# Kernel optimization log

Measured on AMD Instinct MI355X. Metric: run time of the kernel, lower is better.

Reference implementation:

```python
import jax, jax.numpy as jnp
import numpy as np

N_HEADS = 16
D_MODEL = 1024
D_K = D_MODEL // N_HEADS
B, S = 2, 2048


def setup_inputs() -> dict:
    key = jax.random.key(0)
    ks = jax.random.split(key, 12)
    sc = 1.0 / np.sqrt(D_MODEL)
    inp = {
        'query': jax.random.normal(ks[0], (B, S, D_MODEL), jnp.float32),
        'key':   jax.random.normal(ks[1], (B, S, D_MODEL), jnp.float32),
        'value': jax.random.normal(ks[2], (B, S, D_MODEL), jnp.float32),
        'mask':  jnp.ones((B, 1, 1, S), jnp.int32),
        'Wq': jax.random.normal(ks[3], (D_MODEL, D_MODEL), jnp.float32) * sc,
        'bq': jnp.zeros((D_MODEL,), jnp.float32),
        'Wk': jax.random.normal(ks[4], (D_MODEL, D_MODEL), jnp.float32) * sc,
        'bk': jnp.zeros((D_MODEL,), jnp.float32),
        'Wv': jax.random.normal(ks[5], (D_MODEL, D_MODEL), jnp.float32) * sc,
        'bv': jnp.zeros((D_MODEL,), jnp.float32),
        'Wo': jax.random.normal(ks[6], (D_MODEL, D_MODEL), jnp.float32) * sc,
        'bo': jnp.zeros((D_MODEL,), jnp.float32),
    }
    return inp


def reference(query, key, value, mask, Wq, bq, Wk, bk, Wv, bv, Wo, bo):
    # Linear projections (torch Linear: x @ W.T + b)
    q = query @ Wq.T + bq
    k = key @ Wk.T + bk
    v = value @ Wv.T + bv
    # [B, S, D] -> [B, H, S, d_k]
    def split_heads(x):
        b, s, _ = x.shape
        return x.reshape(b, s, N_HEADS, D_K).transpose(0, 2, 1, 3)
    q, k, v = split_heads(q), split_heads(k), split_heads(v)
    # scaled dot-product attention with explicit [B,H,S,S] scores
    att = jnp.einsum('bhqd,bhkd->bhqk', q, k) / jnp.sqrt(jnp.float32(D_K))
    att = jnp.where(mask == 0, -jnp.inf, att)
    scores = jax.nn.softmax(att, axis=-1)
    # dropout is identity in eval/reference mode
    out = jnp.einsum('bhqk,bhkd->bhqd', scores, v)
    b = out.shape[0]
    out = out.transpose(0, 2, 1, 3).reshape(b, -1, N_HEADS * D_K)
    return out @ Wo.T + bo
```

## Files before the change

kernel.cpp:

```cpp
#include <hip/hip_runtime.h>
#include <hip/hip_bf16.h>

#define DM   1024
#define SLEN 2048
#define NH   16
#define DK   64

typedef float f32x4 __attribute__((ext_vector_type(4)));
typedef short short8 __attribute__((ext_vector_type(8)));
typedef short short4v __attribute__((ext_vector_type(4)));

__device__ __forceinline__ unsigned short f2bf(float f) {
  union { float f; unsigned int u; } x; x.f = f;
  unsigned int r = x.u + 0x7fffu + ((x.u >> 16) & 1u);
  return (unsigned short)(r >> 16);
}

__device__ __forceinline__ void gload_lds16(const unsigned short* g, unsigned short* l) {
  __builtin_amdgcn_global_load_lds(
      (const __attribute__((address_space(1))) unsigned int*)g,
      (__attribute__((address_space(3))) unsigned int*)l, 16, 0, 0);
}

__device__ __forceinline__ f32x4 mfma32(short8 a, short8 b, f32x4 c) {
  return __builtin_amdgcn_mfma_f32_16x16x32_bf16(a, b, c, 0, 0, 0);
}

__device__ __forceinline__ f32x4 mfma16(short4v a, short4v b, f32x4 c) {
#if __has_builtin(__builtin_amdgcn_mfma_f32_16x16x16bf16_1k)
  return __builtin_amdgcn_mfma_f32_16x16x16bf16_1k(a, b, c, 0, 0, 0);
#else
  f32x4 d;
  asm volatile("v_mfma_f32_16x16x16_bf16 %0, %1, %2, %3"
               : "=v"(d) : "v"(a), "v"(b), "v"(c));
  return d;
#endif
}

struct ConvArgs { const float* src[7]; unsigned short* dst[7]; };

__global__ __launch_bounds__(256) void conv_kernel(ConvArgs a) {
  int blk = blockIdx.x, seg, base;
  if (blk < 6144) { seg = blk >> 11; base = blk & 2047; }
  else { int t = blk - 6144; seg = 3 + (t >> 9); base = t & 511; }
  const float* s = a.src[seg];
  unsigned short* d = a.dst[seg];
  int idx = (base * 256 + (int)threadIdx.x) * 8;
  float4 v0 = *(const float4*)(s + idx);
  float4 v1 = *(const float4*)(s + idx + 4);
  unsigned short o[8];
  o[0]=f2bf(v0.x); o[1]=f2bf(v0.y); o[2]=f2bf(v0.z); o[3]=f2bf(v0.w);
  o[4]=f2bf(v1.x); o[5]=f2bf(v1.y); o[6]=f2bf(v1.z); o[7]=f2bf(v1.w);
  *(uint4*)(d + idx) = *(uint4*)o;
}

__device__ __forceinline__ void gemm_core(int mode,
                                          const unsigned short* __restrict__ A,
                                          const unsigned short* __restrict__ W,
                                          const float* __restrict__ bias,
                                          void* __restrict__ outp, float scale,
                                          int m0, int n0, char* smem) {
  unsigned short* As = (unsigned short*)smem;
  unsigned short* Bs = (unsigned short*)(smem + 16384);
  const int tid = threadIdx.x;
  const int lane = tid & 63;
  const int l15 = lane & 15;
  const int quad = lane >> 4;
  const int wv = tid >> 6;
  const int wm = (wv >> 1) * 64, wn = (wv & 1) * 32;

  f32x4 acc[4][2];
#pragma unroll
  for (int i = 0; i < 4; ++i)
#pragma unroll
    for (int j = 0; j < 2; ++j) acc[i][j] = (f32x4){0.f, 0.f, 0.f, 0.f};

  for (int k0 = 0; k0 < DM; k0 += 64) {
    __syncthreads();
#pragma unroll
    for (int i = 0; i < 4; ++i) {
      int c = tid + i * 256;
      int row = c >> 3, sc = ((c & 7) ^ (row & 7)) << 3;
      gload_lds16(A + (size_t)(m0 + row) * DM + k0 + sc, As + c * 8);
    }
#pragma unroll
    for (int i = 0; i < 2; ++i) {
      int c = tid + i * 256;
      int row = c >> 3, sc = ((c & 7) ^ (row & 7)) << 3;
      gload_lds16(W + (size_t)(n0 + row) * DM + k0 + sc, Bs + c * 8);
    }
    __syncthreads();
    short8 af[4][2], bf[2][2];
#pragma unroll
    for (int i = 0; i < 4; ++i) {
      int r = wm + i * 16 + l15;
#pragma unroll
      for (int kf = 0; kf < 2; ++kf)
        af[i][kf] = *(const short8*)(As + r * 64 + (((kf * 4 + quad) ^ (r & 7)) << 3));
    }
#pragma unroll
    for (int j = 0; j < 2; ++j) {
      int r = wn + j * 16 + l15;
#pragma unroll
      for (int kf = 0; kf < 2; ++kf)
        bf[j][kf] = *(const short8*)(Bs + r * 64 + (((kf * 4 + quad) ^ (r & 7)) << 3));
    }
#pragma unroll
    for (int kf = 0; kf < 2; ++kf)
#pragma unroll
      for (int i = 0; i < 4; ++i)
#pragma unroll
        for (int j = 0; j < 2; ++j)
          acc[i][j] = mfma32(af[i][kf], bf[j][kf], acc[i][j]);
  }

  const int hh = n0 >> 6;
  const int brow = m0 >> 11;
  const int srow0 = m0 & (SLEN - 1);

  if (mode == 0) {
    __syncthreads();
    unsigned short* Ls = (unsigned short*)smem;
#pragma unroll
    for (int i = 0; i < 4; ++i)
#pragma unroll
      for (int j = 0; j < 2; ++j) {
        int dloc = wn + j * 16 + l15;
        float bv = bias[n0 + dloc];
        int sl = wm + i * 16 + quad * 4;
#pragma unroll
        for (int g = 0; g < 4; ++g)
          Ls[(sl + g) * 66 + dloc] = f2bf((acc[i][j][g] + bv) * scale);
      }
    __syncthreads();
    unsigned short* gout = (unsigned short*)outp +
        ((size_t)(brow * NH + hh) * SLEN + srow0) * DK;
    int sl = tid >> 1, dch = (tid & 1) * 32;
#pragma unroll
    for (int k = 0; k < 4; ++k)
      *(uint4*)(gout + (size_t)sl * DK + dch + k * 8) =
          *(const uint4*)(Ls + sl * 66 + dch + k * 8);
  } else if (mode == 2) {
    __syncthreads();
    unsigned short* Ls = (unsigned short*)smem;
#pragma unroll
    for (int i = 0; i < 4; ++i)
#pragma unroll
      for (int j = 0; j < 2; ++j) {
        int dloc = wn + j * 16 + l15;
        float bv = bias[n0 + dloc];
        int sl = wm + i * 16 + quad * 4;
#pragma unroll
        for (int g = 0; g < 4; ++g)
          Ls[dloc * 132 + sl + g] = f2bf(acc[i][j][g] + bv);
      }
    __syncthreads();
    unsigned short* gout = (unsigned short*)outp +
        (size_t)(brow * NH + hh) * DK * SLEN + srow0;
    int dloc = tid >> 2, sch = (tid & 3) * 32;
#pragma unroll
    for (int k = 0; k < 4; ++k)
      *(uint4*)(gout + (size_t)dloc * SLEN + sch + k * 8) =
          *(const uint4*)(Ls + dloc * 132 + sch + k * 8);
  } else {
    float* Lf = (float*)smem;
#pragma unroll
    for (int hf = 0; hf < 2; ++hf) {
      __syncthreads();
      if ((wv >> 1) == hf) {
#pragma unroll
        for (int i = 0; i < 4; ++i)
#pragma unroll
          for (int j = 0; j < 2; ++j) {
            int dloc = wn + j * 16 + l15;
            float bv = bias[n0 + dloc];
            int sl = i * 16 + quad * 4;
#pragma unroll
            for (int g = 0; g < 4; ++g)
              Lf[(sl + g) * 68 + dloc] = acc[i][j][g] + bv;
          }
      }
      __syncthreads();
      int row = tid >> 2, cch = (tid & 3) * 16;
      float* gout = (float*)outp + (size_t)(m0 + hf * 64 + row) * DM + n0 + cch;
#pragma unroll
      for (int k = 0; k < 4; ++k)
        *(float4*)(gout + k * 4) = *(const float4*)(Lf + row * 68 + cch + k * 4);
    }
  }
}

struct QKVArgs {
  const unsigned short* A[3];
  const unsigned short* W[3];
  const float* bias[3];
  unsigned short* out[3];
  float scale[3];
  int mode[3];
};

__global__ __launch_bounds__(256, 4) void gemm_qkv_kernel(QKVArgs a) {
  __shared__ char smem[24576];
  int z = blockIdx.z, bid = blockIdx.x;
  int xm = (bid & 7) + ((bid >> 7) << 3);
  int yn = (bid >> 3) & 15;
  gemm_core(a.mode[z], a.A[z], a.W[z], a.bias[z], a.out[z], a.scale[z],
            xm * 128, yn * 64, smem);
}

__global__ __launch_bounds__(256, 4) void gemm_o_kernel(const unsigned short* __restrict__ A,
                                                        const unsigned short* __restrict__ W,
                                                        const float* __restrict__ bias,
                                                        float* __restrict__ out) {
  __shared__ char smem[24576];
  int bid = blockIdx.x;
  int xm = (bid & 7) + ((bid >> 7) << 3);
  int yn = (bid >> 3) & 15;
  gemm_core(1, A, W, bias, out, 1.0f, xm * 128, yn * 64, smem);
}

__global__ __launch_bounds__(512, 4) void attn_kernel(
    const unsigned short* __restrict__ Qw,
    const unsigned short* __restrict__ Kw,
    const unsigned short* __restrict__ Vtw,
    const int* __restrict__ mask,
    unsigned short* __restrict__ attn_out) {
  __shared__ uint4 smem4[4160];
  char* smb = (char*)smem4;
  float* Oex = (float*)smb;
  float* lsX = (float*)(smb + 33024);

  const int tid = threadIdx.x;
  const int lane = tid & 63;
  const int l15 = lane & 15;
  const int quad = lane >> 4;
  const int wv = tid >> 6;
  const int grp = wv >> 2;
  const int widx = wv & 3;
  const int tg = tid & 255;

  const int bid = blockIdx.x;
  const int bh = (bid & 7) + ((bid >> 7) << 3);
  const int s0 = ((bid >> 3) & 15) * 128;
  const int b = bh >> 4, h = bh & 15;
  const unsigned short* Qb = Qw + (size_t)bh * (SLEN * DK);
  const unsigned short* Kb = Kw + (size_t)bh * (SLEN * DK);
  const unsigned short* Vtb = Vtw + (size_t)bh * (SLEN * DK);

  const int qb = widx * 32;
  short8 bq[2][2];
#pragma unroll
  for (int qt = 0; qt < 2; ++qt)
#pragma unroll
    for (int kf = 0; kf < 2; ++kf)
      bq[qt][kf] = *(const short8*)(Qb + (size_t)(s0 + qb + qt * 16 + l15) * DK + kf * 32 + quad * 8);

  const int c0 = tg, c1 = tg + 256;
  const int r0c = c0 >> 3, s0c = ((c0 & 7) ^ (r0c & 7)) << 3;
  const int r1c = c1 >> 3, s1c = ((c1 & 7) ^ (r1c & 7)) << 3;

  {
    unsigned short* K0 = (unsigned short*)(smb + grp * 8192);
    unsigned short* V0 = (unsigned short*)(smb + 32768 + grp * 8192);
    int kv0 = grp * 64;
    gload_lds16(Kb + (size_t)(kv0 + r0c) * DK + s0c, K0 + c0 * 8);
    gload_lds16(Kb + (size_t)(kv0 + r1c) * DK + s1c, K0 + c1 * 8);
    gload_lds16(Vtb + (size_t)r0c * SLEN + kv0 + s0c, V0 + c0 * 8);
    gload_lds16(Vtb + (size_t)r1c * SLEN + kv0 + s1c, V0 + c1 * 8);
  }
  int mreg = 1;
  if (tg < 64) {
    ((float*)(smb + 65536 + grp * 256))[tg] = mask[b * SLEN + grp * 64 + tg] ? 0.0f : -1e30f;
    mreg = mask[b * SLEN + (2 + grp) * 64 + tg];
  }
  __syncthreads();

  f32x4 O[4][2];
#pragma unroll
  for (int dt = 0; dt < 4; ++dt)
#pragma unroll
    for (int qt = 0; qt < 2; ++qt) O[dt][qt] = (f32x4){0.f, 0.f, 0.f, 0.f};
  float lsum[2] = {0.f, 0.f};

  int cb = 0;
  for (int it = 0; it < 16; ++it) {
    const int nb = cb ^ 1;
    if (it < 15) {
      unsigned short* Kn = (unsigned short*)(smb + grp * 8192 + nb * 16384);
      unsigned short* Vn = (unsigned short*)(smb + 32768 + grp * 8192 + nb * 16384);
      int kvn = ((it + 1) * 2 + grp) * 64;
      gload_lds16(Kb + (size_t)(kvn + r0c) * DK + s0c, Kn + c0 * 8);
      gload_lds16(Kb + (size_t)(kvn + r1c) * DK + s1c, Kn + c1 * 8);
      gload_lds16(Vtb + (size_t)r0c * SLEN + kvn + s0c, Vn + c0 * 8);
      gload_lds16(Vtb + (size_t)r1c * SLEN + kvn + s1c, Vn + c1 * 8);
      if (tg < 64) {
        ((float*)(smb + 65536 + nb * 512 + grp * 256))[tg] = mreg ? 0.0f : -1e30f;
        if (it < 14) mreg = mask[b * SLEN + ((it + 2) * 2 + grp) * 64 + tg];
      }
    }

    unsigned short* KstG = (unsigned short*)(smb + grp * 8192 + cb * 16384);
    unsigned short* VstG = (unsigned short*)(smb + 32768 + grp * 8192 + cb * 16384);
    float* maskG = (float*)(smb + 65536 + cb * 512 + grp * 256);

    f32x4 st[4][2];
#pragma unroll
    for (int ct = 0; ct < 4; ++ct) {
      int r = ct * 16 + l15;
      short8 ka0 = *(const short8*)(KstG + r * 64 + ((quad ^ (r & 7)) << 3));
      short8 ka1 = *(const short8*)(KstG + r * 64 + (((4 + quad) ^ (r & 7)) << 3));
#pragma unroll
      for (int qt = 0; qt < 2; ++qt) {
        f32x4 z = (f32x4){0.f, 0.f, 0.f, 0.f};
        z = mfma32(ka0, bq[qt][0], z);
        st[ct][qt] = mfma32(ka1, bq[qt][1], z);
      }
    }
    short4v pf[4][2];
#pragma unroll
    for (int ct = 0; ct < 4; ++ct) {
      f32x4 ma = *(const f32x4*)(maskG + ct * 16 + quad * 4);
#pragma unroll
      for (int qt = 0; qt < 2; ++qt) {
        float p0 = __builtin_exp2f(st[ct][qt][0] + ma[0]);
        float p1 = __builtin_exp2f(st[ct][qt][1] + ma[1]);
        float p2 = __builtin_exp2f(st[ct][qt][2] + ma[2]);
        float p3 = __builtin_exp2f(st[ct][qt][3] + ma[3]);
        lsum[qt] += (p0 + p1) + (p2 + p3);
        union { short4v s; __hip_bfloat162 h[2]; } u;
        u.h[0] = __float22bfloat162_rn(float2{p0, p1});
        u.h[1] = __float22bfloat162_rn(float2{p2, p3});
        pf[ct][qt] = u.s;
      }
    }
#pragma unroll
    for (int dt = 0; dt < 4; ++dt) {
      int rd = dt * 16 + l15;
      short4v vf[4];
#pragma unroll
      for (int ct = 0; ct < 4; ++ct) {
        int slot = (ct * 2 + (quad >> 1)) ^ (rd & 7);
        vf[ct] = *(const short4v*)(VstG + rd * 64 + slot * 8 + (quad & 1) * 4);
      }
#pragma unroll
      for (int qt = 0; qt < 2; ++qt)
#pragma unroll
        for (int ct = 0; ct < 4; ++ct)
          O[dt][qt] = mfma16(vf[ct], pf[ct][qt], O[dt][qt]);
    }
    __syncthreads();
    cb = nb;
  }

#pragma unroll
  for (int qt = 0; qt < 2; ++qt) {
    lsum[qt] += __shfl_xor(lsum[qt], 16);
    lsum[qt] += __shfl_xor(lsum[qt], 32);
  }
  if (grp == 1) {
#pragma unroll
    for (int dt = 0; dt < 4; ++dt)
#pragma unroll
      for (int qt = 0; qt < 2; ++qt) {
        int qg = qb + qt * 16 + l15;
#pragma unroll
        for (int i = 0; i < 4; ++i)
          Oex[(dt * 16 + quad * 4 + i) * 129 + qg] = O[dt][qt][i];
      }
    if (quad == 0) {
      lsX[qb + lane] = lsum[0];
      lsX[qb + 16 + lane] = lsum[1];
    }
  }
  __syncthreads();
  if (grp == 0) {
#pragma unroll
    for (int qt = 0; qt < 2; ++qt) {
      int qg = qb + qt * 16 + l15;
      float inv = 1.0f / (lsum[qt] + lsX[qg]);
      int srow = s0 + qg;
#pragma unroll
      for (int dt = 0; dt < 4; ++dt) {
        int d0 = dt * 16 + quad * 4;
        unsigned short pk[4];
#pragma unroll
        for (int i = 0; i < 4; ++i)
          pk[i] = f2bf((O[dt][qt][i] + Oex[(d0 + i) * 129 + qg]) * inv);
        *(uint2*)(attn_out + (size_t)(b * SLEN + srow) * DM + h * DK + d0) = *(uint2*)pk;
      }
    }
  }
}

extern "C" void kernel_launch(void* const* d_in, const int* in_sizes, int n_in,
                              void* d_out, int out_size, void* d_ws, size_t ws_size,
                              hipStream_t stream) {
  (void)in_sizes; (void)n_in; (void)out_size; (void)ws_size;
  const float* query = (const float*)d_in[0];
  const float* key_  = (const float*)d_in[1];
  const float* value = (const float*)d_in[2];
  const int*   mask  = (const int*)d_in[3];
  const float* Wq = (const float*)d_in[4];
  const float* bq = (const float*)d_in[5];
  const float* Wk = (const float*)d_in[6];
  const float* bk = (const float*)d_in[7];
  const float* Wv = (const float*)d_in[8];
  const float* bv = (const float*)d_in[9];
  const float* Wo = (const float*)d_in[10];
  const float* bo = (const float*)d_in[11];
  float* out = (float*)d_out;

  const size_t WSZ = 1048576, XSZ = 4194304;
  unsigned short* base = (unsigned short*)d_ws;
  unsigned short* Wqb = base;
  unsigned short* Wkb = base + WSZ;
  unsigned short* Wvb = base + 2 * WSZ;
  unsigned short* Wob = base + 3 * WSZ;
  unsigned short* Xqb = base + 4 * WSZ;
  unsigned short* Xkb = Xqb + XSZ;
  unsigned short* Xvb = Xqb + 2 * XSZ;
  unsigned short* Qw  = Xqb + 3 * XSZ;
  unsigned short* Kw  = Qw + XSZ;
  unsigned short* Vtw = Qw + 2 * XSZ;
  unsigned short* attnb = Qw + 3 * XSZ;

  ConvArgs ca;
  ca.src[0] = query; ca.src[1] = key_; ca.src[2] = value;
  ca.src[3] = Wq; ca.src[4] = Wk; ca.src[5] = Wv; ca.src[6] = Wo;
  ca.dst[0] = Xqb; ca.dst[1] = Xkb; ca.dst[2] = Xvb;
  ca.dst[3] = Wqb; ca.dst[4] = Wkb; ca.dst[5] = Wvb; ca.dst[6] = Wob;
  conv_kernel<<<8192, 256, 0, stream>>>(ca);

  QKVArgs qa;
  qa.A[0] = Xqb; qa.A[1] = Xkb; qa.A[2] = Xvb;
  qa.W[0] = Wqb; qa.W[1] = Wkb; qa.W[2] = Wvb;
  qa.bias[0] = bq; qa.bias[1] = bk; qa.bias[2] = bv;
  qa.out[0] = Qw; qa.out[1] = Kw; qa.out[2] = Vtw;
  qa.scale[0] = 0.18033688011112042f;
  qa.scale[1] = 1.0f; qa.scale[2] = 1.0f;
  qa.mode[0] = 0; qa.mode[1] = 0; qa.mode[2] = 2;
  gemm_qkv_kernel<<<dim3(512, 1, 3), 256, 0, stream>>>(qa);

  attn_kernel<<<dim3(512), 512, 0, stream>>>(Qw, Kw, Vtw, mask, attnb);

  gemm_o_kernel<<<dim3(512), 256, 0, stream>>>(attnb, Wob, bo, out);
}
```

Measured before the change: 250.6 us.

## Enlarge GEMM tiles to 128x128, shrink K-step, and register-stage attention K/V loads

```diff
diff --git a/kernel.cpp b/kernel.cpp
--- a/kernel.cpp
+++ b/kernel.cpp
@@ -61,131 +61,129 @@
                                           void* __restrict__ outp, float scale,
                                           int m0, int n0, char* smem) {
   unsigned short* As = (unsigned short*)smem;
-  unsigned short* Bs = (unsigned short*)(smem + 16384);
+  unsigned short* Bs = (unsigned short*)(smem + 8192);
   const int tid = threadIdx.x;
   const int lane = tid & 63;
   const int l15 = lane & 15;
   const int quad = lane >> 4;
   const int wv = tid >> 6;
-  const int wm = (wv >> 1) * 64, wn = (wv & 1) * 32;
-
-  f32x4 acc[4][2];
+  const int wm = (wv >> 1) * 64, wn = (wv & 1) * 64;
+
+  f32x4 acc[4][4];
 #pragma unroll
   for (int i = 0; i < 4; ++i)
 #pragma unroll
-    for (int j = 0; j < 2; ++j) acc[i][j] = (f32x4){0.f, 0.f, 0.f, 0.f};
-
-  for (int k0 = 0; k0 < DM; k0 += 64) {
+    for (int j = 0; j < 4; ++j) acc[i][j] = (f32x4){0.f, 0.f, 0.f, 0.f};
+
+  const int crow = tid >> 2, coff = (tid & 3) << 3;
+  const int crow2 = (tid + 256) >> 2, coff2 = ((tid + 256) & 3) << 3;
+
+  for (int k0 = 0; k0 < DM; k0 += 32) {
     __syncthreads();
-#pragma unroll
-    for (int i = 0; i < 4; ++i) {
-      int c = tid + i * 256;
-      int row = c >> 3, sc = ((c & 7) ^ (row & 7)) << 3;
-      gload_lds16(A + (size_t)(m0 + row) * DM + k0 + sc, As + c * 8);
-    }
-#pragma unroll
-    for (int i = 0; i < 2; ++i) {
-      int c = tid + i * 256;
-      int row = c >> 3, sc = ((c & 7) ^ (row & 7)) << 3;
-      gload_lds16(W + (size_t)(n0 + row) * DM + k0 + sc, Bs + c * 8);
-    }
+    gload_lds16(A + (size_t)(m0 + crow) * DM + k0 + coff, As + tid * 8);
+    gload_lds16(A + (size_t)(m0 + crow2) * DM + k0 + coff2, As + (tid + 256) * 8);
+    gload_lds16(W + (size_t)(n0 + crow) * DM + k0 + coff, Bs + tid * 8);
+    gload_lds16(W + (size_t)(n0 + crow2) * DM + k0 + coff2, Bs + (tid + 256) * 8);
     __syncthreads();
-    short8 af[4][2], bf[2][2];
-#pragma unroll
-    for (int i = 0; i < 4; ++i) {
-      int r = wm + i * 16 + l15;
-#pragma unroll
-      for (int kf = 0; kf < 2; ++kf)
-        af[i][kf] = *(const short8*)(As + r * 64 + (((kf * 4 + quad) ^ (r & 7)) << 3));
-    }
-#pragma unroll
-    for (int j = 0; j < 2; ++j) {
-      int r = wn + j * 16 + l15;
-#pragma unroll
-      for (int kf = 0; kf < 2; ++kf)
-        bf[j][kf] = *(const short8*)(Bs + r * 64 + (((kf * 4 + quad) ^ (r & 7)) << 3));
-    }
-#pragma unroll
-    for (int kf = 0; kf < 2; ++kf)
-#pragma unroll
-      for (int i = 0; i < 4; ++i)
-#pragma unroll
-        for (int j = 0; j < 2; ++j)
-          acc[i][j] = mfma32(af[i][kf], bf[j][kf], acc[i][j]);
-  }
-
-  const int hh = n0 >> 6;
+    short8 af[4], bf[4];
+#pragma unroll
+    for (int i = 0; i < 4; ++i)
+      af[i] = *(const short8*)(As + (wm + i * 16 + l15) * 32 + quad * 8);
+#pragma unroll
+    for (int j = 0; j < 4; ++j)
+      bf[j] = *(const short8*)(Bs + (wn + j * 16 + l15) * 32 + quad * 8);
+#pragma unroll
+    for (int i = 0; i < 4; ++i)
+#pragma unroll
+      for (int j = 0; j < 4; ++j)
+        acc[i][j] = mfma32(af[i], bf[j], acc[i][j]);
+  }
+
   const int brow = m0 >> 11;
   const int srow0 = m0 & (SLEN - 1);
 
   if (mode == 0) {
-    __syncthreads();
     unsigned short* Ls = (unsigned short*)smem;
 #pragma unroll
-    for (int i = 0; i < 4; ++i)
-#pragma unroll
-      for (int j = 0; j < 2; ++j) {
-        int dloc = wn + j * 16 + l15;
-        float bv = bias[n0 + dloc];
-        int sl = wm + i * 16 + quad * 4;
-#pragma unroll
-        for (int g = 0; g < 4; ++g)
-          Ls[(sl + g) * 66 + dloc] = f2bf((acc[i][j][g] + bv) * scale);
-      }
-    __syncthreads();
-    unsigned short* gout = (unsigned short*)outp +
-        ((size_t)(brow * NH + hh) * SLEN + srow0) * DK;
-    int sl = tid >> 1, dch = (tid & 1) * 32;
-#pragma unroll
-    for (int k = 0; k < 4; ++k)
-      *(uint4*)(gout + (size_t)sl * DK + dch + k * 8) =
-          *(const uint4*)(Ls + sl * 66 + dch + k * 8);
+    for (int hf = 0; hf < 2; ++hf) {
+      __syncthreads();
+      if ((wv & 1) == hf) {
+#pragma unroll
+        for (int i = 0; i < 4; ++i)
+#pragma unroll
+          for (int j = 0; j < 4; ++j) {
+            int dloc = j * 16 + l15;
+            float bv = bias[n0 + hf * 64 + dloc];
+            int sl = wm + i * 16 + quad * 4;
+#pragma unroll
+            for (int g = 0; g < 4; ++g)
+              Ls[(sl + g) * 66 + dloc] = f2bf((acc[i][j][g] + bv) * scale);
+          }
+      }
+      __syncthreads();
+      int head = (n0 >> 6) + hf;
+      unsigned short* gout = (unsigned short*)outp +
+          ((size_t)(brow * NH + head) * SLEN + srow0) * DK;
+      int sl = tid >> 1, dch = (tid & 1) * 32;
+#pragma unroll
+      for (int k = 0; k < 4; ++k)
+        *(uint4*)(gout + (size_t)sl * DK + dch + k * 8) =
+            *(const uint4*)(Ls + sl * 66 + dch + k * 8);
+    }
   } else if (mode == 2) {
-    __syncthreads();
     unsigned short* Ls = (unsigned short*)smem;
 #pragma unroll
-    for (int i = 0; i < 4; ++i)
-#pragma unroll
-      for (int j = 0; j < 2; ++j) {
-        int dloc = wn + j * 16 + l15;
-        float bv = bias[n0 + dloc];
-        int sl = wm + i * 16 + quad * 4;
-#pragma unroll
-        for (int g = 0; g < 4; ++g)
-          Ls[dloc * 132 + sl + g] = f2bf(acc[i][j][g] + bv);
-      }
-    __syncthreads();
-    unsigned short* gout = (unsigned short*)outp +
-        (size_t)(brow * NH + hh) * DK * SLEN + srow0;
-    int dloc = tid >> 2, sch = (tid & 3) * 32;
-#pragma unroll
-    for (int k = 0; k < 4; ++k)
-      *(uint4*)(gout + (size_t)dloc * SLEN + sch + k * 8) =
-          *(const uint4*)(Ls + dloc * 132 + sch + k * 8);
+    for (int hf = 0; hf < 2; ++hf) {
+      __syncthreads();
+      if ((wv & 1) == hf) {
+#pragma unroll
+        for (int i = 0; i < 4; ++i)
+#pragma unroll
+          for (int j = 0; j < 4; ++j) {
+            int dloc = j * 16 + l15;
+            float bv = bias[n0 + hf * 64 + dloc];
+            int sl = wm + i * 16 + quad * 4;
+#pragma unroll
+            for (int g = 0; g < 4; ++g)
+              Ls[dloc * 132 + sl + g] = f2bf(acc[i][j][g] + bv);
+          }
+      }
+      __syncthreads();
+      int head = (n0 >> 6) + hf;
+      unsigned short* gout = (unsigned short*)outp +
+          (size_t)(brow * NH + head) * DK * SLEN + srow0;
+      int dloc = tid >> 2, sch = (tid & 3) * 32;
+#pragma unroll
+      for (int k = 0; k < 4; ++k)
+        *(uint4*)(gout + (size_t)dloc * SLEN + sch + k * 8) =
+            *(const uint4*)(Ls + dloc * 132 + sch + k * 8);
+    }
   } else {
     float* Lf = (float*)smem;
 #pragma unroll
-    for (int hf = 0; hf < 2; ++hf) {
-      __syncthreads();
-      if ((wv >> 1) == hf) {
-#pragma unroll
-        for (int i = 0; i < 4; ++i)
-#pragma unroll
-          for (int j = 0; j < 2; ++j) {
-            int dloc = wn + j * 16 + l15;
-            float bv = bias[n0 + dloc];
-            int sl = i * 16 + quad * 4;
+    for (int hf = 0; hf < 4; ++hf) {
+      __syncthreads();
+      if ((wv >> 1) == (hf >> 1)) {
+#pragma unroll
+        for (int ii = 0; ii < 2; ++ii) {
+          int i = (hf & 1) * 2 + ii;
+#pragma unroll
+          for (int j = 0; j < 4; ++j) {
+            int cloc = wn + j * 16 + l15;
+            float bv = bias[n0 + cloc];
+            int lr = ii * 16 + quad * 4;
 #pragma unroll
             for (int g = 0; g < 4; ++g)
-              Lf[(sl + g) * 68 + dloc] = acc[i][j][g] + bv;
+              Lf[(lr + g) * 132 + cloc] = acc[i][j][g] + bv;
           }
-      }
-      __syncthreads();
-      int row = tid >> 2, cch = (tid & 3) * 16;
-      float* gout = (float*)outp + (size_t)(m0 + hf * 64 + row) * DM + n0 + cch;
+        }
+      }
+      __syncthreads();
+      int row = tid >> 3, cch = (tid & 7) * 16;
+      float* gout = (float*)outp + (size_t)(m0 + hf * 32 + row) * DM + n0 + cch;
 #pragma unroll
       for (int k = 0; k < 4; ++k)
-        *(float4*)(gout + k * 4) = *(const float4*)(Lf + row * 68 + cch + k * 4);
+        *(float4*)(gout + k * 4) = *(const float4*)(Lf + row * 132 + cch + k * 4);
     }
   }
 }
@@ -199,24 +197,24 @@
   int mode[3];
 };
 
-__global__ __launch_bounds__(256, 4) void gemm_qkv_kernel(QKVArgs a) {
-  __shared__ char smem[24576];
-  int z = blockIdx.z, bid = blockIdx.x;
-  int xm = (bid & 7) + ((bid >> 7) << 3);
-  int yn = (bid >> 3) & 15;
+__global__ __launch_bounds__(256, 3) void gemm_qkv_kernel(QKVArgs a) {
+  __shared__ char smem[17408];
+  int z = blockIdx.z, x = blockIdx.x;
+  int xm = (x & 7) | (((x >> 3) & 3) << 3);
+  int yn = x >> 5;
   gemm_core(a.mode[z], a.A[z], a.W[z], a.bias[z], a.out[z], a.scale[z],
-            xm * 128, yn * 64, smem);
-}
-
-__global__ __launch_bounds__(256, 4) void gemm_o_kernel(const unsigned short* __restrict__ A,
+            xm * 128, yn * 128, smem);
+}
+
+__global__ __launch_bounds__(256, 3) void gemm_o_kernel(const unsigned short* __restrict__ A,
                                                         const unsigned short* __restrict__ W,
                                                         const float* __restrict__ bias,
                                                         float* __restrict__ out) {
-  __shared__ char smem[24576];
-  int bid = blockIdx.x;
-  int xm = (bid & 7) + ((bid >> 7) << 3);
-  int yn = (bid >> 3) & 15;
-  gemm_core(1, A, W, bias, out, 1.0f, xm * 128, yn * 64, smem);
+  __shared__ char smem[17408];
+  int x = blockIdx.x;
+  int xm = (x & 7) | (((x >> 3) & 3) << 3);
+  int yn = x >> 5;
+  gemm_core(1, A, W, bias, out, 1.0f, xm * 128, yn * 128, smem);
 }
 
 __global__ __launch_bounds__(512, 4) void attn_kernel(
@@ -225,7 +223,7 @@
     const unsigned short* __restrict__ Vtw,
     const int* __restrict__ mask,
     unsigned short* __restrict__ attn_out) {
-  __shared__ uint4 smem4[4160];
+  __shared__ uint4 smem4[2336];
   char* smb = (char*)smem4;
   float* Oex = (float*)smb;
   float* lsX = (float*)(smb + 33024);
@@ -247,6 +245,10 @@
   const unsigned short* Kb = Kw + (size_t)bh * (SLEN * DK);
   const unsigned short* Vtb = Vtw + (size_t)bh * (SLEN * DK);
 
+  unsigned short* Kst = (unsigned short*)(smb + grp * 9216);
+  unsigned short* Vst = (unsigned short*)(smb + 18432 + grp * 9216);
+  float* maskG = (float*)(smb + 36864 + grp * 256);
+
   const int qb = widx * 32;
   short8 bq[2][2];
 #pragma unroll
@@ -256,22 +258,29 @@
       bq[qt][kf] = *(const short8*)(Qb + (size_t)(s0 + qb + qt * 16 + l15) * DK + kf * 32 + quad * 8);
 
   const int c0 = tg, c1 = tg + 256;
-  const int r0c = c0 >> 3, s0c = ((c0 & 7) ^ (r0c & 7)) << 3;
-  const int r1c = c1 >> 3, s1c = ((c1 & 7) ^ (r1c & 7)) << 3;
-
+  const int r0c = c0 >> 3, o0c = (c0 & 7) << 3;
+  const int r1c = c1 >> 3, o1c = (c1 & 7) << 3;
+
+  uint4 kreg[2], vreg[2];
+  int mreg;
   {
-    unsigned short* K0 = (unsigned short*)(smb + grp * 8192);
-    unsigned short* V0 = (unsigned short*)(smb + 32768 + grp * 8192);
     int kv0 = grp * 64;
-    gload_lds16(Kb + (size_t)(kv0 + r0c) * DK + s0c, K0 + c0 * 8);
-    gload_lds16(Kb + (size_t)(kv0 + r1c) * DK + s1c, K0 + c1 * 8);
-    gload_lds16(Vtb + (size_t)r0c * SLEN + kv0 + s0c, V0 + c0 * 8);
-    gload_lds16(Vtb + (size_t)r1c * SLEN + kv0 + s1c, V0 + c1 * 8);
-  }
-  int mreg = 1;
-  if (tg < 64) {
-    ((float*)(smb + 65536 + grp * 256))[tg] = mask[b * SLEN + grp * 64 + tg] ? 0.0f : -1e30f;
-    mreg = mask[b * SLEN + (2 + grp) * 64 + tg];
+    kreg[0] = *(const uint4*)(Kb + (size_t)(kv0 + r0c) * DK + o0c);
+    kreg[1] = *(const uint4*)(Kb + (size_t)(kv0 + r1c) * DK + o1c);
+    vreg[0] = *(const uint4*)(Vtb + (size_t)r0c * SLEN + kv0 + o0c);
+    vreg[1] = *(const uint4*)(Vtb + (size_t)r1c * SLEN + kv0 + o1c);
+    int m0r = (tg < 64) ? mask[b * SLEN + kv0 + tg] : 1;
+    *(uint4*)(Kst + r0c * 72 + o0c) = kreg[0];
+    *(uint4*)(Kst + r1c * 72 + o1c) = kreg[1];
+    *(uint4*)(Vst + r0c * 72 + o0c) = vreg[0];
+    *(uint4*)(Vst + r1c * 72 + o1c) = vreg[1];
+    if (tg < 64) maskG[tg] = m0r ? 0.0f : -1e30f;
+    int kv1 = (2 + grp) * 64;
+    kreg[0] = *(const uint4*)(Kb + (size_t)(kv1 + r0c) * DK + o0c);
+    kreg[1] = *(const uint4*)(Kb + (size_t)(kv1 + r1c) * DK + o1c);
+    vreg[0] = *(const uint4*)(Vtb + (size_t)r0c * SLEN + kv1 + o0c);
+    vreg[1] = *(const uint4*)(Vtb + (size_t)r1c * SLEN + kv1 + o1c);
+    mreg = (tg < 64) ? mask[b * SLEN + kv1 + tg] : 1;
   }
   __syncthreads();
 
@@ -282,33 +291,13 @@
     for (int qt = 0; qt < 2; ++qt) O[dt][qt] = (f32x4){0.f, 0.f, 0.f, 0.f};
   float lsum[2] = {0.f, 0.f};
 
-  int cb = 0;
   for (int it = 0; it < 16; ++it) {
-    const int nb = cb ^ 1;
-    if (it < 15) {
-      unsigned short* Kn = (unsigned short*)(smb + grp * 8192 + nb * 16384);
-      unsigned short* Vn = (unsigned short*)(smb + 32768 + grp * 8192 + nb * 16384);
-      int kvn = ((it + 1) * 2 + grp) * 64;
-      gload_lds16(Kb + (size_t)(kvn + r0c) * DK + s0c, Kn + c0 * 8);
-      gload_lds16(Kb + (size_t)(kvn + r1c) * DK + s1c, Kn + c1 * 8);
-      gload_lds16(Vtb + (size_t)r0c * SLEN + kvn + s0c, Vn + c0 * 8);
-      gload_lds16(Vtb + (size_t)r1c * SLEN + kvn + s1c, Vn + c1 * 8);
-      if (tg < 64) {
-        ((float*)(smb + 65536 + nb * 512 + grp * 256))[tg] = mreg ? 0.0f : -1e30f;
-        if (it < 14) mreg = mask[b * SLEN + ((it + 2) * 2 + grp) * 64 + tg];
-      }
-    }
-
-    unsigned short* KstG = (unsigned short*)(smb + grp * 8192 + cb * 16384);
-    unsigned short* VstG = (unsigned short*)(smb + 32768 + grp * 8192 + cb * 16384);
-    float* maskG = (float*)(smb + 65536 + cb * 512 + grp * 256);
-
     f32x4 st[4][2];
 #pragma unroll
     for (int ct = 0; ct < 4; ++ct) {
       int r = ct * 16 + l15;
-      short8 ka0 = *(const short8*)(KstG + r * 64 + ((quad ^ (r & 7)) << 3));
-      short8 ka1 = *(const short8*)(KstG + r * 64 + (((4 + quad) ^ (r & 7)) << 3));
+      short8 ka0 = *(const short8*)(Kst + r * 72 + quad * 8);
+      short8 ka1 = *(const short8*)(Kst + r * 72 + 32 + quad * 8);
 #pragma unroll
       for (int qt = 0; qt < 2; ++qt) {
         f32x4 z = (f32x4){0.f, 0.f, 0.f, 0.f};
@@ -338,10 +327,8 @@
       int rd = dt * 16 + l15;
       short4v vf[4];
 #pragma unroll
-      for (int ct = 0; ct < 4; ++ct) {
-        int slot = (ct * 2 + (quad >> 1)) ^ (rd & 7);
-        vf[ct] = *(const short4v*)(VstG + rd * 64 + slot * 8 + (quad & 1) * 4);
-      }
+      for (int ct = 0; ct < 4; ++ct)
+        vf[ct] = *(const short4v*)(Vst + rd * 72 + ct * 16 + quad * 4);
 #pragma unroll
       for (int qt = 0; qt < 2; ++qt)
 #pragma unroll
@@ -349,7 +336,22 @@
           O[dt][qt] = mfma16(vf[ct], pf[ct][qt], O[dt][qt]);
     }
     __syncthreads();
-    cb = nb;
+    if (it < 15) {
+      *(uint4*)(Kst + r0c * 72 + o0c) = kreg[0];
+      *(uint4*)(Kst + r1c * 72 + o1c) = kreg[1];
+      *(uint4*)(Vst + r0c * 72 + o0c) = vreg[0];
+      *(uint4*)(Vst + r1c * 72 + o1c) = vreg[1];
+      if (tg < 64) maskG[tg] = mreg ? 0.0f : -1e30f;
+      if (it < 14) {
+        int kvn = ((it + 2) * 2 + grp) * 64;
+        kreg[0] = *(const uint4*)(Kb + (size_t)(kvn + r0c) * DK + o0c);
+        kreg[1] = *(const uint4*)(Kb + (size_t)(kvn + r1c) * DK + o1c);
+        vreg[0] = *(const uint4*)(Vtb + (size_t)r0c * SLEN + kvn + o0c);
+        vreg[1] = *(const uint4*)(Vtb + (size_t)r1c * SLEN + kvn + o1c);
+        mreg = (tg < 64) ? mask[b * SLEN + kvn + tg] : 1;
+      }
+      __syncthreads();
+    }
   }
 
 #pragma unroll
@@ -357,6 +359,7 @@
     lsum[qt] += __shfl_xor(lsum[qt], 16);
     lsum[qt] += __shfl_xor(lsum[qt], 32);
   }
+  __syncthreads();
   if (grp == 1) {
 #pragma unroll
     for (int dt = 0; dt < 4; ++dt)
@@ -439,9 +442,9 @@
   qa.scale[0] = 0.18033688011112042f;
   qa.scale[1] = 1.0f; qa.scale[2] = 1.0f;
   qa.mode[0] = 0; qa.mode[1] = 0; qa.mode[2] = 2;
-  gemm_qkv_kernel<<<dim3(512, 1, 3), 256, 0, stream>>>(qa);
+  gemm_qkv_kernel<<<dim3(256, 1, 3), 256, 0, stream>>>(qa);
 
   attn_kernel<<<dim3(512), 512, 0, stream>>>(Qw, Kw, Vtw, mask, attnb);
 
-  gemm_o_kernel<<<dim3(512), 256, 0, stream>>>(attnb, Wob, bo, out);
-}
+  gemm_o_kernel<<<dim3(256), 256, 0, stream>>>(attnb, Wob, bo, out);
+}
```

Result: slower. 323.5 us (+29.1%).
